# Kernel tuning notes

Measured on AMD Instinct MI355X. Metric: run time of the kernel, lower is better.

The kernel has to match this reference:

```python
import jax, jax.numpy as jnp
import numpy as np

NUM_HEADS = 8
BN_EPS = 1e-3  # keras BatchNormalization default epsilon


def setup_inputs() -> dict:
    key = jax.random.key(0)
    ks = jax.random.split(key, 4)
    B, N, C, s, H = 8, 1024, 3, 16, NUM_HEADS
    dim = s * s * C  # 768
    return {
        "x": jax.random.normal(ks[0], (B, N, dim), jnp.float32),
        "qconv_w": jax.random.normal(ks[1], (3, 3, C, C), jnp.float32) * 0.1,  # HWIO, shared q/k/v (source bug, faithful)
        "reatten_w": jax.random.normal(ks[2], (H, H), jnp.float32) * 0.2,      # 1x1 conv mixing heads
        "reatten_b": jnp.zeros((H,), jnp.float32),
        "bn_gamma": jnp.ones((H,), jnp.float32),
        "bn_beta": jnp.zeros((H,), jnp.float32),
        "bn_mean": jnp.zeros((H,), jnp.float32),
        "bn_var": jnp.ones((H,), jnp.float32),
        "proj_w": jax.random.normal(ks[3], (dim, dim), jnp.float32) * 0.02,
        "proj_b": jnp.zeros((dim,), jnp.float32),
    }


def reference(x, qconv_w, reatten_w, reatten_b, bn_gamma, bn_beta, bn_mean, bn_var, proj_w, proj_b):
    H = NUM_HEADS
    B, N, P = x.shape
    C = qconv_w.shape[2]
    s = int(np.sqrt(P // C))
    hd = P // H
    scale = hd ** -0.5

    # unflatten: tokens become conv batch; 3x3 same conv, no bias
    xim = x.reshape(B * N, s, s, C)
    y = jax.lax.conv_general_dilated(
        xim, qconv_w, window_strides=(1, 1), padding='SAME',
        dimension_numbers=('NHWC', 'HWIO', 'NHWC'))
    # source applies qconv2d for q, k AND v -> identical projections
    q = y.reshape(B, N, H, hd).transpose(0, 2, 1, 3)  # [B,H,N,hd]

    attn = jax.nn.softmax(jnp.einsum('bhnd,bhmd->bhnm', q, q) * scale, axis=-1)

    # re-attention: 1x1 conv across heads + inference batchnorm (per head channel), reatten_scale=1.0
    re = jnp.einsum('bhnm,hg->bgnm', attn, reatten_w) + reatten_b[None, :, None, None]
    st = lambda a: a[None, :, None, None]
    attn_next = (re - st(bn_mean)) * st(bn_gamma) / jnp.sqrt(st(bn_var) + BN_EPS) + st(bn_beta)

    out = jnp.einsum('bgnm,bgmd->bngd', attn_next, q).reshape(B, N, P)
    xo = out @ proj_w + proj_b
    return (xo, attn_next)
```

## Files before the change

kernel.cpp:

```cpp
#include <hip/hip_runtime.h>

#define NB 8
#define NN 1024
#define NH 8
#define HD 96
#define DIM 768

typedef __bf16 bf16x8 __attribute__((ext_vector_type(8)));
typedef float f32x4 __attribute__((ext_vector_type(4)));
typedef unsigned short u16x8 __attribute__((ext_vector_type(8)));
typedef _Float16 half8 __attribute__((ext_vector_type(8)));

__device__ __forceinline__ ushort f2bf(float f) {
  uint u = __float_as_uint(f);
  u += 0x7fffu + ((u >> 16) & 1u);
  return (ushort)(u >> 16);
}
__device__ __forceinline__ float bf2f(ushort u) {
  return __uint_as_float(((uint)u) << 16);
}
__device__ __forceinline__ ushort f2h(float f) {
  union { _Float16 h; ushort u; } c;
  c.h = (_Float16)f;
  return c.u;
}

__global__ __launch_bounds__(256) void k_prep_w(const float* __restrict__ pw,
                                                ushort* __restrict__ wT) {
  __shared__ ushort tile[64][72];
  int d0 = blockIdx.x * 64;
  int j0 = blockIdx.y * 64;
  int t = threadIdx.x;
  {
    int r = t >> 2;
    int ch = (t & 3) * 16;
    const float* src = pw + (size_t)(d0 + r) * DIM + j0 + ch;
#pragma unroll
    for (int i = 0; i < 16; i += 4) {
      float4 v = *(const float4*)(src + i);
      tile[ch + i + 0][r] = f2bf(v.x);
      tile[ch + i + 1][r] = f2bf(v.y);
      tile[ch + i + 2][r] = f2bf(v.z);
      tile[ch + i + 3][r] = f2bf(v.w);
    }
  }
  __syncthreads();
  {
    int j = t >> 2;
    int ch = (t & 3) * 16;
    union { ushort u[16]; uint4 v[2]; } tmp;
#pragma unroll
    for (int i = 0; i < 16; ++i) tmp.u[i] = tile[j][ch + i];
    uint4* dst = (uint4*)(wT + (size_t)(j0 + j) * DIM + d0 + ch);
    dst[0] = tmp.v[0]; dst[1] = tmp.v[1];
  }
}

__global__ __launch_bounds__(256) void k_conv(const float* __restrict__ x,
                                              const float* __restrict__ w,
                                              ushort* __restrict__ q) {
  __shared__ float xs[768];
  __shared__ float ws[81];
  __shared__ ushort os[768];
  int token = blockIdx.x;
  int t = threadIdx.x;
  const float4* xin = (const float4*)(x + (size_t)token * DIM);
  if (t < 192) ((float4*)xs)[t] = xin[t];
  if (t < 81) ws[t] = w[t];
  __syncthreads();
  int r = t >> 4, c = t & 15;
  float a0 = 0.f, a1 = 0.f, a2 = 0.f;
#pragma unroll
  for (int dr = 0; dr < 3; ++dr) {
    int rr = r + dr - 1;
    bool rok = (rr >= 0) & (rr < 16);
#pragma unroll
    for (int dc = 0; dc < 3; ++dc) {
      int cc = c + dc - 1;
      bool ok = rok & (cc >= 0) & (cc < 16);
#pragma unroll
      for (int ci = 0; ci < 3; ++ci) {
        int idx = ok ? (rr * 16 + cc) * 3 + ci : 0;
        float xv = xs[idx];
        xv = ok ? xv : 0.f;
        const float* wp = ws + ((dr * 3 + dc) * 3 + ci) * 3;
        a0 += xv * wp[0]; a1 += xv * wp[1]; a2 += xv * wp[2];
      }
    }
  }
  os[t * 3 + 0] = f2bf(a0);
  os[t * 3 + 1] = f2bf(a1);
  os[t * 3 + 2] = f2bf(a2);
  __syncthreads();
  uint4* dst = (uint4*)(q + (size_t)token * DIM);
  if (t < 96) dst[t] = ((const uint4*)os)[t];
}

__global__ __launch_bounds__(256) void k_transpose_q(const ushort* __restrict__ q,
                                                     ushort* __restrict__ qT) {
  __shared__ ushort tile[64][72];
  int bb = blockIdx.z;
  int n0 = blockIdx.x * 64;
  int d0 = blockIdx.y * 64;
  int t = threadIdx.x;
  {
    int r = t >> 2;
    int cq = (t & 3) * 16;
    const ushort* src = q + ((size_t)(bb * NN) + n0 + r) * DIM + d0 + cq;
    uint4 v0 = *(const uint4*)src;
    uint4 v1 = *(const uint4*)(src + 8);
    *(uint4*)&tile[r][cq] = v0;
    *(uint4*)&tile[r][cq + 8] = v1;
  }
  __syncthreads();
  {
    int d = t >> 2;
    int nch = (t & 3) * 16;
    union { ushort u[16]; uint4 v[2]; } tmp;
#pragma unroll
    for (int j = 0; j < 16; ++j) tmp.u[j] = tile[nch + j][d];
    uint4* dst = (uint4*)(qT + ((size_t)(bb * DIM) + d0 + d) * NN + n0 + nch);
    dst[0] = tmp.v[0]; dst[1] = tmp.v[1];
  }
}

__global__ __launch_bounds__(256) void k_qk(const ushort* __restrict__ q,
                                            ushort* __restrict__ p,
                                            float* __restrict__ psum, int b0) {
  __shared__ ushort As[128][104];
  __shared__ ushort Bs[128][104];
  __shared__ float rsum_l[128][2];
  int z = blockIdx.z;
  int bc = z >> 3, h = z & 7;
  int bb = b0 + bc;
  int r0 = blockIdx.x * 128;
  int c0 = blockIdx.y * 128;
  int t = threadIdx.x;
  const ushort* qb = q + (size_t)bb * NN * DIM + h * HD;
  for (int i = t; i < 1536; i += 256) {
    int row = i / 12;
    int ck = (i % 12) * 8;
    *(uint4*)&As[row][ck] = *(const uint4*)(qb + (size_t)(r0 + row) * DIM + ck);
    *(uint4*)&Bs[row][ck] = *(const uint4*)(qb + (size_t)(c0 + row) * DIM + ck);
  }
  __syncthreads();
  int wv = t >> 6, lane = t & 63;
  int wr = (wv >> 1) * 64, wc = (wv & 1) * 64;
  int lm = lane & 15, lg = lane >> 4;
  f32x4 acc[4][4] = {};
#pragma unroll
  for (int ks = 0; ks < 3; ++ks) {
    bf16x8 af[4], bfr[4];
#pragma unroll
    for (int mi = 0; mi < 4; ++mi)
      af[mi] = *(const bf16x8*)&As[wr + mi * 16 + lm][ks * 32 + lg * 8];
#pragma unroll
    for (int ni = 0; ni < 4; ++ni)
      bfr[ni] = *(const bf16x8*)&Bs[wc + ni * 16 + lm][ks * 32 + lg * 8];
#pragma unroll
    for (int mi = 0; mi < 4; ++mi)
#pragma unroll
      for (int ni = 0; ni < 4; ++ni)
        acc[mi][ni] = __builtin_amdgcn_mfma_f32_16x16x32_bf16(af[mi], bfr[ni], acc[mi][ni], 0, 0, 0);
  }
  const float scale = 0.10206207261596575f;
  ushort* pb = p + (size_t)(bc * 8 + h) * NN * NN;
  float rsum[4][4] = {};
#pragma unroll
  for (int mi = 0; mi < 4; ++mi)
#pragma unroll
    for (int ni = 0; ni < 4; ++ni)
#pragma unroll
      for (int r = 0; r < 4; ++r) {
        float e = __expf(acc[mi][ni][r] * scale);
        int row = r0 + wr + mi * 16 + lg * 4 + r;
        int col = c0 + wc + ni * 16 + lm;
        pb[(size_t)row * NN + col] = f2h(e);
        rsum[mi][r] += e;
      }
#pragma unroll
  for (int mi = 0; mi < 4; ++mi)
#pragma unroll
    for (int r = 0; r < 4; ++r) {
      float s = rsum[mi][r];
      s += __shfl_xor(s, 1); s += __shfl_xor(s, 2);
      s += __shfl_xor(s, 4); s += __shfl_xor(s, 8);
      if (lm == 0) rsum_l[wr + mi * 16 + lg * 4 + r][wv & 1] = s;
    }
  __syncthreads();
  if (t < 128)
    psum[((size_t)(bc * 8 + h) * 8 + blockIdx.y) * NN + r0 + t] =
        rsum_l[t][0] + rsum_l[t][1];
}

__global__ __launch_bounds__(256) void k_inv(const float* __restrict__ psum,
                                             float* __restrict__ invb, int b0) {
  int gi = blockIdx.x * 256 + threadIdx.x;
  int bhc = gi >> 10, n = gi & 1023;
  float s = 0.f;
#pragma unroll
  for (int cb = 0; cb < 8; ++cb) s += psum[((size_t)bhc * 8 + cb) * NN + n];
  invb[(size_t)(b0 * 8 + bhc) * NN + n] = 1.f / s;
}

__global__ __launch_bounds__(512, 4) void k_mixpv(
    const ushort* __restrict__ p, const ushort* __restrict__ qT,
    const float* __restrict__ invb, const float* __restrict__ rw,
    const float* __restrict__ rb, const float* __restrict__ gamma,
    const float* __restrict__ beta, const float* __restrict__ mean,
    const float* __restrict__ var,
    float* __restrict__ attn, ushort* __restrict__ outb,
    int b0, int bmask, int bshift) {
  __shared__ char P[2][16384];

  const int lin = blockIdx.x;
  const int bc = lin & bmask;
  const int bb = b0 + bc;
  const int nt = lin >> bshift;
  const int n0 = nt * 16;
  const int t = threadIdx.x;
  const int w = t >> 6, lane = t & 63;
  const int lm = lane & 15, lg = lane >> 4;

  float coef[8];
#pragma unroll
  for (int h = 0; h < 8; ++h)
    coef[h] = rw[h * 8 + w] * invb[(size_t)(bb * 8 + h) * NN + n0 + lm];
  const float effs = gamma[w] * __frsqrt_rn(var[w] + 1e-3f);
  const float effb = (rb[w] - mean[w]) * effs + beta[w];

  const ushort* pb = p + (size_t)bc * 8 * NN * NN;
  const ushort* vb = qT + (size_t)bb * DIM * NN;

  const int srow = t >> 2, q4 = t & 3;
  const int sh_ = srow >> 4, sn = srow & 15;
  const int swz_s = (sn & 7) << 4;
  const ushort* psrc = pb + ((size_t)(sh_ * NN) + n0 + sn) * NN + q4 * 16;

  f32x4 oacc[6] = {};

  {
    uint4 u0 = *(const uint4*)(psrc);
    uint4 u1 = *(const uint4*)(psrc + 8);
    char* base = P[0] + srow * 128;
    *(uint4*)(base + ((q4 * 32) ^ swz_s)) = u0;
    *(uint4*)(base + ((q4 * 32 + 16) ^ swz_s)) = u1;
  }
  __syncthreads();

  for (int mt = 0; mt < 16; ++mt) {
    if (mt < 15) {
      const ushort* sp = psrc + (mt + 1) * 64;
      uint4 u0 = *(const uint4*)(sp);
      uint4 u1 = *(const uint4*)(sp + 8);
      char* base = P[(mt + 1) & 1] + srow * 128;
      *(uint4*)(base + ((q4 * 32) ^ swz_s)) = u0;
      *(uint4*)(base + ((q4 * 32 + 16) ^ swz_s)) = u1;
    }
    const char* Pc = P[mt & 1];
    const int m0 = mt * 64;
#pragma unroll
    for (int ks = 0; ks < 2; ++ks) {
      float mix[8];
#pragma unroll
      for (int j = 0; j < 8; ++j) mix[j] = 0.f;
      const int cb = (ks * 64 + lg * 16) ^ ((lm & 7) << 4);
#pragma unroll
      for (int h = 0; h < 8; ++h) {
        union { u16x8 u; half8 hh; } pu;
        pu.u = *(const u16x8*)(Pc + (h * 16 + lm) * 128 + cb);
        float c = coef[h];
#pragma unroll
        for (int j = 0; j < 8; ++j) mix[j] += (float)pu.hh[j] * c;
      }
      f32x4 o0, o1;
#pragma unroll
      for (int j = 0; j < 4; ++j) o0[j] = mix[j] * effs + effb;
#pragma unroll
      for (int j = 0; j < 4; ++j) o1[j] = mix[4 + j] * effs + effb;
      size_t arow = ((size_t)(bb * 8 + w) * NN + (n0 + lm)) * NN + m0 + ks * 32 + lg * 8;
      __builtin_nontemporal_store(o0, (f32x4*)(attn + arow));
      __builtin_nontemporal_store(o1, (f32x4*)(attn + arow + 4));
      u16x8 pk;
#pragma unroll
      for (int j = 0; j < 4; ++j) pk[j] = f2bf(o0[j]);
#pragma unroll
      for (int j = 0; j < 4; ++j) pk[4 + j] = f2bf(o1[j]);
      bf16x8 pmf = *(bf16x8*)&pk;
      bf16x8 vf[6];
#pragma unroll
      for (int df = 0; df < 6; ++df)
        vf[df] = *(const bf16x8*)(vb + (size_t)(w * HD + df * 16 + lm) * NN
                                   + m0 + ks * 32 + lg * 8);
#pragma unroll
      for (int df = 0; df < 6; ++df)
        oacc[df] = __builtin_amdgcn_mfma_f32_16x16x32_bf16(pmf, vf[df], oacc[df], 0, 0, 0);
    }
    __syncthreads();
  }

#pragma unroll
  for (int df = 0; df < 6; ++df) {
    int col = w * HD + df * 16 + lm;
#pragma unroll
    for (int r = 0; r < 4; ++r) {
      int row = n0 + lg * 4 + r;
      outb[(size_t)(bb * NN + row) * DIM + col] = f2bf(oacc[df][r]);
    }
  }
}

__global__ __launch_bounds__(256) void k_proj(const ushort* __restrict__ outb,
                                              const ushort* __restrict__ wT,
                                              const float* __restrict__ pb,
                                              float* __restrict__ xo) {
  __shared__ ushort As[128][72];
  __shared__ ushort Bs[128][72];
  int m0 = blockIdx.x * 128;
  int j0 = blockIdx.y * 128;
  int t = threadIdx.x;
  int wv = t >> 6, lane = t & 63;
  int wr = (wv >> 1) * 64, wc = (wv & 1) * 64;
  int lm = lane & 15, lg = lane >> 4;
  f32x4 acc[4][4] = {};
  for (int kk = 0; kk < 12; ++kk) {
    int k0 = kk * 64;
    __syncthreads();
    for (int i = t; i < 1024; i += 256) {
      int row = i >> 3;
      int c = (i & 7) * 8;
      *(uint4*)&As[row][c] = *(const uint4*)(outb + (size_t)(m0 + row) * DIM + k0 + c);
      *(uint4*)&Bs[row][c] = *(const uint4*)(wT + (size_t)(j0 + row) * DIM + k0 + c);
    }
    __syncthreads();
#pragma unroll
    for (int ks = 0; ks < 2; ++ks) {
      bf16x8 af[4], bfr[4];
#pragma unroll
      for (int mi = 0; mi < 4; ++mi)
        af[mi] = *(const bf16x8*)&As[wr + mi * 16 + lm][ks * 32 + lg * 8];
#pragma unroll
      for (int ni = 0; ni < 4; ++ni)
        bfr[ni] = *(const bf16x8*)&Bs[wc + ni * 16 + lm][ks * 32 + lg * 8];
#pragma unroll
      for (int mi = 0; mi < 4; ++mi)
#pragma unroll
        for (int ni = 0; ni < 4; ++ni)
          acc[mi][ni] = __builtin_amdgcn_mfma_f32_16x16x32_bf16(af[mi], bfr[ni], acc[mi][ni], 0, 0, 0);
    }
  }
#pragma unroll
  for (int ni = 0; ni < 4; ++ni) {
    int col = j0 + wc + ni * 16 + lm;
    float bias = pb[col];
#pragma unroll
    for (int mi = 0; mi < 4; ++mi)
#pragma unroll
      for (int r = 0; r < 4; ++r) {
        int row = m0 + wr + mi * 16 + lg * 4 + r;
        xo[(size_t)row * DIM + col] = acc[mi][ni][r] + bias;
      }
  }
}

extern "C" void kernel_launch(void* const* d_in, const int* in_sizes, int n_in,
                              void* d_out, int out_size, void* d_ws, size_t ws_size,
                              hipStream_t stream) {
  (void)in_sizes; (void)n_in; (void)out_size;
  const float* x       = (const float*)d_in[0];
  const float* qconv_w = (const float*)d_in[1];
  const float* rw      = (const float*)d_in[2];
  const float* rb      = (const float*)d_in[3];
  const float* gamma   = (const float*)d_in[4];
  const float* beta    = (const float*)d_in[5];
  const float* mean    = (const float*)d_in[6];
  const float* var     = (const float*)d_in[7];
  const float* pw      = (const float*)d_in[8];
  const float* pb      = (const float*)d_in[9];

  float* xo   = (float*)d_out;
  float* attn = xo + (size_t)NB * NN * DIM;

  char* ws = (char*)d_ws;
  ushort* q    = (ushort*)(ws);
  ushort* qT   = (ushort*)(ws + 12582912);
  ushort* wT   = (ushort*)(ws + 25165824);
  ushort* outb = (ushort*)(ws + 26345472);
  float*  invb = (float*)(ws + 38928384);
  float*  psum = (float*)(ws + 39190528);
  ushort* p    = (ushort*)(ws + 41287680);

  hipLaunchKernelGGL(k_prep_w, dim3(12, 12), dim3(256), 0, stream, pw, wT);
  hipLaunchKernelGGL(k_conv, dim3(NB * NN), dim3(256), 0, stream, x, qconv_w, q);
  hipLaunchKernelGGL(k_transpose_q, dim3(16, 12, NB), dim3(256), 0, stream, q, qT);

  if (ws_size >= 175505408ull) {
    hipLaunchKernelGGL(k_qk, dim3(8, 8, 64), dim3(256), 0, stream, q, p, psum, 0);
    hipLaunchKernelGGL(k_inv, dim3(256), dim3(256), 0, stream, psum, invb, 0);
    hipLaunchKernelGGL(k_mixpv, dim3(512), dim3(512), 0, stream, p, qT, invb,
                       rw, rb, gamma, beta, mean, var, attn, outb, 0, 7, 3);
  } else {
    for (int c = 0; c < NB; ++c) {
      hipLaunchKernelGGL(k_qk, dim3(8, 8, 8), dim3(256), 0, stream, q, p, psum, c);
      hipLaunchKernelGGL(k_inv, dim3(32), dim3(256), 0, stream, psum, invb, c);
      hipLaunchKernelGGL(k_mixpv, dim3(64), dim3(512), 0, stream, p, qT, invb,
                         rw, rb, gamma, beta, mean, var, attn, outb, c, 0, 0);
    }
  }
  hipLaunchKernelGGL(k_proj, dim3(64, 6), dim3(256), 0, stream, outb, wT, pb, xo);
}
```

Baseline: 252.8 us.

## Split mixpv key dimension in halves with atomic fp32 accumulation

Splits the key (m) range of the mix+PV kernel into two halves, doubling the block count to 1024 so more of the GPU is occupied. Partial outputs are accumulated with float atomics into a zeroed fp32 buffer, and a new kernel then converts the result to bf16 for the projection. The price is a memset, atomic traffic, an extra pass over a 25 MB buffer and a larger workspace requirement, which may push some configurations onto the chunked fallback path.

New measurement: 282.9 us. +11.9%, slower.

```diff
diff --git a/kernel.cpp b/kernel.cpp
--- a/kernel.cpp
+++ b/kernel.cpp
@@ -209,15 +209,18 @@
     const float* __restrict__ rb, const float* __restrict__ gamma,
     const float* __restrict__ beta, const float* __restrict__ mean,
     const float* __restrict__ var,
-    float* __restrict__ attn, ushort* __restrict__ outb,
+    float* __restrict__ attn, float* __restrict__ pacc,
     int b0, int bmask, int bshift) {
   __shared__ char P[2][16384];
 
   const int lin = blockIdx.x;
   const int bc = lin & bmask;
   const int bb = b0 + bc;
-  const int nt = lin >> bshift;
+  const int rest = lin >> bshift;
+  const int nt = rest >> 1;
+  const int mh = rest & 1;
   const int n0 = nt * 16;
+  const int mbase = mh * 512;
   const int t = threadIdx.x;
   const int w = t >> 6, lane = t & 63;
   const int lm = lane & 15, lg = lane >> 4;
@@ -235,7 +238,7 @@
   const int srow = t >> 2, q4 = t & 3;
   const int sh_ = srow >> 4, sn = srow & 15;
   const int swz_s = (sn & 7) << 4;
-  const ushort* psrc = pb + ((size_t)(sh_ * NN) + n0 + sn) * NN + q4 * 16;
+  const ushort* psrc = pb + ((size_t)(sh_ * NN) + n0 + sn) * NN + mbase + q4 * 16;
 
   f32x4 oacc[6] = {};
 
@@ -248,8 +251,8 @@
   }
   __syncthreads();
 
-  for (int mt = 0; mt < 16; ++mt) {
-    if (mt < 15) {
+  for (int mt = 0; mt < 8; ++mt) {
+    if (mt < 7) {
       const ushort* sp = psrc + (mt + 1) * 64;
       uint4 u0 = *(const uint4*)(sp);
       uint4 u1 = *(const uint4*)(sp + 8);
@@ -258,7 +261,7 @@
       *(uint4*)(base + ((q4 * 32 + 16) ^ swz_s)) = u1;
     }
     const char* Pc = P[mt & 1];
-    const int m0 = mt * 64;
+    const int m0 = mbase + mt * 64;
 #pragma unroll
     for (int ks = 0; ks < 2; ++ks) {
       float mix[8];
@@ -305,9 +308,18 @@
 #pragma unroll
     for (int r = 0; r < 4; ++r) {
       int row = n0 + lg * 4 + r;
-      outb[(size_t)(bb * NN + row) * DIM + col] = f2bf(oacc[df][r]);
-    }
-  }
+      unsafeAtomicAdd(&pacc[(size_t)(bc * NN + row) * DIM + col], oacc[df][r]);
+    }
+  }
+}
+
+__global__ __launch_bounds__(256) void k_sumfix(const float* __restrict__ pacc,
+                                                ushort* __restrict__ outb) {
+  size_t base = ((size_t)blockIdx.x * 256 + threadIdx.x) * 4;
+  f32x4 v = *(const f32x4*)(pacc + base);
+  ushort4 o;
+  o.x = f2bf(v[0]); o.y = f2bf(v[1]); o.z = f2bf(v[2]); o.w = f2bf(v[3]);
+  *(ushort4*)(outb + base) = o;
 }
 
 __global__ __launch_bounds__(256) void k_proj(const ushort* __restrict__ outb,
@@ -388,23 +400,29 @@
   ushort* outb = (ushort*)(ws + 26345472);
   float*  invb = (float*)(ws + 38928384);
   float*  psum = (float*)(ws + 39190528);
-  ushort* p    = (ushort*)(ws + 41287680);
-
+  float*  pacc = (float*)(ws + 41287680);
   hipLaunchKernelGGL(k_prep_w, dim3(12, 12), dim3(256), 0, stream, pw, wT);
   hipLaunchKernelGGL(k_conv, dim3(NB * NN), dim3(256), 0, stream, x, qconv_w, q);
   hipLaunchKernelGGL(k_transpose_q, dim3(16, 12, NB), dim3(256), 0, stream, q, qT);
 
-  if (ws_size >= 175505408ull) {
+  if (ws_size >= 200671232ull) {
+    ushort* p = (ushort*)(ws + 66453504);
+    hipMemsetAsync(pacc, 0, (size_t)NB * NN * DIM * sizeof(float), stream);
     hipLaunchKernelGGL(k_qk, dim3(8, 8, 64), dim3(256), 0, stream, q, p, psum, 0);
     hipLaunchKernelGGL(k_inv, dim3(256), dim3(256), 0, stream, psum, invb, 0);
-    hipLaunchKernelGGL(k_mixpv, dim3(512), dim3(512), 0, stream, p, qT, invb,
-                       rw, rb, gamma, beta, mean, var, attn, outb, 0, 7, 3);
+    hipLaunchKernelGGL(k_mixpv, dim3(1024), dim3(512), 0, stream, p, qT, invb,
+                       rw, rb, gamma, beta, mean, var, attn, pacc, 0, 7, 3);
+    hipLaunchKernelGGL(k_sumfix, dim3(6144), dim3(256), 0, stream, pacc, outb);
   } else {
+    ushort* p = (ushort*)(ws + 44433408);
     for (int c = 0; c < NB; ++c) {
+      hipMemsetAsync(pacc, 0, (size_t)NN * DIM * sizeof(float), stream);
       hipLaunchKernelGGL(k_qk, dim3(8, 8, 8), dim3(256), 0, stream, q, p, psum, c);
       hipLaunchKernelGGL(k_inv, dim3(32), dim3(256), 0, stream, psum, invb, c);
-      hipLaunchKernelGGL(k_mixpv, dim3(64), dim3(512), 0, stream, p, qT, invb,
-                         rw, rb, gamma, beta, mean, var, attn, outb, c, 0, 0);
+      hipLaunchKernelGGL(k_mixpv, dim3(128), dim3(512), 0, stream, p, qT, invb,
+                         rw, rb, gamma, beta, mean, var, attn, pacc, c, 0, 0);
+      hipLaunchKernelGGL(k_sumfix, dim3(768), dim3(256), 0, stream, pacc,
+                         outb + (size_t)c * NN * DIM);
     }
   }
   hipLaunchKernelGGL(k_proj, dim3(64, 6), dim3(256), 0, stream, outb, wT, pb, xo);
```

## Drop LDS reduction in k_qk and double P tile width in k_mixpv

Applied to the files above, without the earlier changes.

k_qk now writes per-wave partial row sums directly to global psum, with twice as many partials, instead of combining the two column-waves through shared memory behind a barrier. k_inv is changed to sum 16 partials. Separately, k_mixpv stages 128-column P tiles instead of 64, which halves the outer loop iterations and barriers but doubles LDS use to 64KB per block. That may limit occupancy under launch_bounds(512,4). The workspace offsets and the size threshold are adjusted to make room for the larger psum.

After: 252.4 us. No clear change (-0.1%).

```diff
diff --git a/kernel.cpp b/kernel.cpp
--- a/kernel.cpp
+++ b/kernel.cpp
@@ -129,7 +129,6 @@
                                             float* __restrict__ psum, int b0) {
   __shared__ ushort As[128][104];
   __shared__ ushort Bs[128][104];
-  __shared__ float rsum_l[128][2];
   int z = blockIdx.z;
   int bc = z >> 3, h = z & 7;
   int bb = b0 + bc;
@@ -178,6 +177,7 @@
         pb[(size_t)row * NN + col] = f2h(e);
         rsum[mi][r] += e;
       }
+  float* ps = psum + ((size_t)((bc * 8 + h) * 8 + blockIdx.y) * 2 + (wv & 1)) * NN + r0;
 #pragma unroll
   for (int mi = 0; mi < 4; ++mi)
 #pragma unroll
@@ -185,12 +185,8 @@
       float s = rsum[mi][r];
       s += __shfl_xor(s, 1); s += __shfl_xor(s, 2);
       s += __shfl_xor(s, 4); s += __shfl_xor(s, 8);
-      if (lm == 0) rsum_l[wr + mi * 16 + lg * 4 + r][wv & 1] = s;
-    }
-  __syncthreads();
-  if (t < 128)
-    psum[((size_t)(bc * 8 + h) * 8 + blockIdx.y) * NN + r0 + t] =
-        rsum_l[t][0] + rsum_l[t][1];
+      if (lm == 0) ps[wr + mi * 16 + lg * 4 + r] = s;
+    }
 }
 
 __global__ __launch_bounds__(256) void k_inv(const float* __restrict__ psum,
@@ -199,7 +195,7 @@
   int bhc = gi >> 10, n = gi & 1023;
   float s = 0.f;
 #pragma unroll
-  for (int cb = 0; cb < 8; ++cb) s += psum[((size_t)bhc * 8 + cb) * NN + n];
+  for (int cb = 0; cb < 16; ++cb) s += psum[((size_t)bhc * 16 + cb) * NN + n];
   invb[(size_t)(b0 * 8 + bhc) * NN + n] = 1.f / s;
 }
 
@@ -211,7 +207,7 @@
     const float* __restrict__ var,
     float* __restrict__ attn, ushort* __restrict__ outb,
     int b0, int bmask, int bshift) {
-  __shared__ char P[2][16384];
+  __shared__ char P[2][32768];
 
   const int lin = blockIdx.x;
   const int bc = lin & bmask;
@@ -235,40 +231,43 @@
   const int srow = t >> 2, q4 = t & 3;
   const int sh_ = srow >> 4, sn = srow & 15;
   const int swz_s = (sn & 7) << 4;
-  const ushort* psrc = pb + ((size_t)(sh_ * NN) + n0 + sn) * NN + q4 * 16;
+  const ushort* psrc = pb + ((size_t)(sh_ * NN) + n0 + sn) * NN + q4 * 32;
 
   f32x4 oacc[6] = {};
 
   {
-    uint4 u0 = *(const uint4*)(psrc);
-    uint4 u1 = *(const uint4*)(psrc + 8);
-    char* base = P[0] + srow * 128;
-    *(uint4*)(base + ((q4 * 32) ^ swz_s)) = u0;
-    *(uint4*)(base + ((q4 * 32 + 16) ^ swz_s)) = u1;
-  }
-  __syncthreads();
-
-  for (int mt = 0; mt < 16; ++mt) {
-    if (mt < 15) {
-      const ushort* sp = psrc + (mt + 1) * 64;
-      uint4 u0 = *(const uint4*)(sp);
-      uint4 u1 = *(const uint4*)(sp + 8);
-      char* base = P[(mt + 1) & 1] + srow * 128;
-      *(uint4*)(base + ((q4 * 32) ^ swz_s)) = u0;
-      *(uint4*)(base + ((q4 * 32 + 16) ^ swz_s)) = u1;
+    char* base = P[0] + srow * 256;
+#pragma unroll
+    for (int i = 0; i < 4; ++i) {
+      uint4 u = *(const uint4*)(psrc + i * 8);
+      *(uint4*)(base + ((q4 * 64 + i * 16) ^ swz_s)) = u;
+    }
+  }
+  __syncthreads();
+
+  for (int mt = 0; mt < 8; ++mt) {
+    if (mt < 7) {
+      const ushort* sp = psrc + (mt + 1) * 128;
+      char* base = P[(mt + 1) & 1] + srow * 256;
+#pragma unroll
+      for (int i = 0; i < 4; ++i) {
+        uint4 u = *(const uint4*)(sp + i * 8);
+        *(uint4*)(base + ((q4 * 64 + i * 16) ^ swz_s)) = u;
+      }
     }
     const char* Pc = P[mt & 1];
-    const int m0 = mt * 64;
-#pragma unroll
-    for (int ks = 0; ks < 2; ++ks) {
+    const int m0 = mt * 128;
+#pragma unroll
+    for (int ks = 0; ks < 4; ++ks) {
       float mix[8];
 #pragma unroll
       for (int j = 0; j < 8; ++j) mix[j] = 0.f;
-      const int cb = (ks * 64 + lg * 16) ^ ((lm & 7) << 4);
+      const int cb = (ks * 32 + lg * 8) * 2;
+      const int cbs = cb ^ ((lm & 7) << 4);
 #pragma unroll
       for (int h = 0; h < 8; ++h) {
         union { u16x8 u; half8 hh; } pu;
-        pu.u = *(const u16x8*)(Pc + (h * 16 + lm) * 128 + cb);
+        pu.u = *(const u16x8*)(Pc + (h * 16 + lm) * 256 + cbs);
         float c = coef[h];
 #pragma unroll
         for (int j = 0; j < 8; ++j) mix[j] += (float)pu.hh[j] * c;
@@ -388,13 +387,13 @@
   ushort* outb = (ushort*)(ws + 26345472);
   float*  invb = (float*)(ws + 38928384);
   float*  psum = (float*)(ws + 39190528);
-  ushort* p    = (ushort*)(ws + 41287680);
+  ushort* p    = (ushort*)(ws + 43384832);
 
   hipLaunchKernelGGL(k_prep_w, dim3(12, 12), dim3(256), 0, stream, pw, wT);
   hipLaunchKernelGGL(k_conv, dim3(NB * NN), dim3(256), 0, stream, x, qconv_w, q);
   hipLaunchKernelGGL(k_transpose_q, dim3(16, 12, NB), dim3(256), 0, stream, q, qT);
 
-  if (ws_size >= 175505408ull) {
+  if (ws_size >= 177602560ull) {
     hipLaunchKernelGGL(k_qk, dim3(8, 8, 64), dim3(256), 0, stream, q, p, psum, 0);
     hipLaunchKernelGGL(k_inv, dim3(256), dim3(256), 0, stream, psum, invb, 0);
     hipLaunchKernelGGL(k_mixpv, dim3(512), dim3(512), 0, stream, p, qT, invb,
```
